# Optimization experiments

Hardware: AMD Instinct MI355X
Metric: run time of the kernel (lower is better)

Reference implementation:

```python
import jax, jax.numpy as jnp
import numpy as np
from jax import lax

B, T, F = 8, 512, 128          # batch, mel time, mel freq
DM, DS, DC, EXP, NL = 384, 16, 4, 2, 12
DI = EXP * DM                   # 768 inner width
DTR = (DM + 15) // 16           # 24, mamba_ssm dt_rank='auto'
PT = PF = 16
L = (T // PT) * (F // PF)       # 256 patches
NC = 4


def setup_inputs() -> dict:
    key = jax.random.key(0)
    ks = iter(jax.random.split(key, 24))
    def n(shape, s=0.02):
        return jax.random.normal(next(ks), shape, jnp.float32) * s
    return {
        "x": jax.random.normal(next(ks), (B, T, F), jnp.float32),
        "patch_w": n((DM, PT, PF)),
        "patch_b": jnp.zeros((DM,), jnp.float32),
        "pos_embed": n((1, L, DM)),
        "ln_g": jnp.ones((NL, DM), jnp.float32),
        "ln_b": jnp.zeros((NL, DM), jnp.float32),
        "in_proj_w": n((NL, 2 * DI, DM)),
        "conv_w": n((NL, DI, DC), 0.1),
        "conv_b": jnp.zeros((NL, DI), jnp.float32),
        "x_proj_w": n((NL, DTR + 2 * DS, DI)),
        "dt_proj_w": n((NL, DI, DTR), 0.1),
        "dt_proj_b": n((NL, DI), 0.1),
        "A_log": jnp.tile(jnp.log(jnp.arange(1, DS + 1, dtype=jnp.float32))[None, None, :], (NL, DI, 1)),
        "Dskip": jnp.ones((NL, DI), jnp.float32),
        "out_proj_w": n((NL, DM, DI)),
        "fn_g": jnp.ones((DM,), jnp.float32),
        "fn_b": jnp.zeros((DM,), jnp.float32),
        "head_w": n((NC, DM)),
        "head_b": jnp.zeros((NC,), jnp.float32),
    }


def _layernorm(x, g, b):
    m = x.mean(-1, keepdims=True)
    v = jnp.var(x, axis=-1, keepdims=True)
    return (x - m) * lax.rsqrt(v + 1e-5) * g + b


def _silu(v):
    return v * jax.nn.sigmoid(v)


def _mamba_block(x, p):
    # x: [B, L, DM]; residual Mamba block (pre-LN, dropout=identity in eval)
    ln_g, ln_b, Wi, cw, cb, Wx, Wdt, bdt, A_log, Dsk, Wo = p
    res = x
    h = _layernorm(x, ln_g, ln_b)
    xz = jnp.einsum('bld,ed->ble', h, Wi)          # [B,L,2*DI]
    u, z = jnp.split(xz, 2, axis=-1)
    # causal depthwise conv1d, kernel DC (small, unrolled)
    up = jnp.pad(u, ((0, 0), (DC - 1, 0), (0, 0)))
    u = sum(up[:, k:k + L, :] * cw[:, k] for k in range(DC)) + cb
    u = _silu(u)
    proj = jnp.einsum('bld,ed->ble', u, Wx)        # [B,L,DTR+2*DS]
    dt, Bm, Cm = jnp.split(proj, [DTR, DTR + DS], axis=-1)
    delta = jax.nn.softplus(jnp.einsum('blr,dr->bld', dt, Wdt) + bdt)  # [B,L,DI]
    A = -jnp.exp(A_log)                            # [DI, DS]
    dA = jnp.exp(delta[..., None] * A)             # [B,L,DI,DS]
    dBu = (delta * u)[..., None] * Bm[:, :, None, :]

    def step(hst, inp):
        dA_t, dBu_t, C_t = inp
        hst = dA_t * hst + dBu_t                   # [B,DI,DS]
        return hst, jnp.einsum('bdn,bn->bd', hst, C_t)

    h0 = jnp.zeros((x.shape[0], DI, DS), x.dtype)
    _, ys = lax.scan(step, h0, (dA.swapaxes(0, 1), dBu.swapaxes(0, 1), Cm.swapaxes(0, 1)))
    y = ys.swapaxes(0, 1) + u * Dsk                # [B,L,DI]
    y = y * _silu(z)
    return res + jnp.einsum('bld,ed->ble', y, Wo)


def reference(x, patch_w, patch_b, pos_embed, ln_g, ln_b, in_proj_w, conv_w, conv_b,
              x_proj_w, dt_proj_w, dt_proj_b, A_log, Dskip, out_proj_w,
              fn_g, fn_b, head_w, head_b):
    Bn = x.shape[0]
    # patch embed = non-overlapping 16x16 conv == blocked reshape + einsum
    patches = x.reshape(Bn, T // PT, PT, F // PF, PF)
    tok = jnp.einsum('bhpwq,dpq->bhwd', patches, patch_w) + patch_b
    tok = tok.reshape(Bn, L, DM) + pos_embed

    def layer(carry, p):
        return _mamba_block(carry, p), None

    tok, _ = lax.scan(layer, tok, (ln_g, ln_b, in_proj_w, conv_w, conv_b,
                                   x_proj_w, dt_proj_w, dt_proj_b, A_log, Dskip, out_proj_w))
    tok = _layernorm(tok, fn_g, fn_b)
    pooled = tok.mean(axis=1)
    return pooled @ head_w.T + head_b
```

## Files before the change

kernel.cpp:

```cpp
#include <hip/hip_runtime.h>
#include <math.h>

namespace {

constexpr int kB   = 8;
constexpr int kL   = 256;
constexpr int kTok = 2048;
constexpr int kDM  = 384;
constexpr int kDI  = 768;
constexpr int kDS  = 16;
constexpr int kDTR = 24;
constexpr int kPROJ = 56;
constexpr int kNL  = 12;

constexpr int kWIN  = 2 * kDI * kDM;
constexpr int kWOUT = kDM * kDI;
constexpr int kWX   = kPROJ * kDI;
constexpr int kWTOT = kWIN + kWOUT + kWX;

typedef float f32x4 __attribute__((ext_vector_type(4)));
typedef short short8 __attribute__((ext_vector_type(8)));

__device__ __forceinline__ float softplus_f(float x) {
  return (x > 20.f) ? x : log1pf(__expf(x));
}
__device__ __forceinline__ float silu_f(float x) {
  return x / (1.f + __expf(-x));
}
__device__ __forceinline__ unsigned short f2bf(float f) {
  union { float f; unsigned u; } v; v.f = f;
  unsigned r = v.u + 0x7FFFu + ((v.u >> 16) & 1u);
  return (unsigned short)(r >> 16);
}
__device__ __forceinline__ float bf2f(unsigned short u) {
  return __uint_as_float((unsigned)u << 16);
}

__global__ __launch_bounds__(256) void patch_gemm_k(
    const float* __restrict__ x, const float* __restrict__ Bw,
    const float* __restrict__ bias, const float* __restrict__ pos,
    float* __restrict__ C) {
  __shared__ float As[16][68];
  __shared__ float Bs[16][68];
  int tid = threadIdx.x;
  int bm = blockIdx.y * 64;
  int bn = blockIdx.x * 64;
  int lr = tid >> 2;
  int lk = (tid & 3) << 2;
  int tm = (tid >> 4) << 2;
  int tn = (tid & 15) << 2;
  float acc[4][4] = {};
  for (int k0 = 0; k0 < 256; k0 += 16) {
    {
      int token = bm + lr;
      int b = token >> 8, l = token & 255;
      int h = l >> 3, w = l & 7;
      int p = k0 >> 4;
      const float* ap = x + ((size_t)(b * 512) + h * 16 + p) * 128 + w * 16 + lk;
      float4 av = *(const float4*)ap;
      As[lk + 0][lr] = av.x; As[lk + 1][lr] = av.y;
      As[lk + 2][lr] = av.z; As[lk + 3][lr] = av.w;
    }
    {
      const float* bp = Bw + (size_t)(bn + lr) * 256 + k0 + lk;
      float4 bv = *(const float4*)bp;
      Bs[lk + 0][lr] = bv.x; Bs[lk + 1][lr] = bv.y;
      Bs[lk + 2][lr] = bv.z; Bs[lk + 3][lr] = bv.w;
    }
    __syncthreads();
    #pragma unroll
    for (int k = 0; k < 16; ++k) {
      float4 a = *(const float4*)&As[k][tm];
      float4 b = *(const float4*)&Bs[k][tn];
      float av[4] = {a.x, a.y, a.z, a.w};
      float bv[4] = {b.x, b.y, b.z, b.w};
      #pragma unroll
      for (int i = 0; i < 4; ++i)
        #pragma unroll
        for (int j = 0; j < 4; ++j)
          acc[i][j] = fmaf(av[i], bv[j], acc[i][j]);
    }
    __syncthreads();
  }
  #pragma unroll
  for (int i = 0; i < 4; ++i) {
    int row = bm + tm + i;
    #pragma unroll
    for (int j = 0; j < 4; ++j) {
      int col = bn + tn + j;
      C[(size_t)row * kDM + col] =
          acc[i][j] + bias[col] + pos[(size_t)(row & 255) * kDM + col];
    }
  }
}

__global__ __launch_bounds__(384) void lnpool_head_k(
    const float* __restrict__ in, const float* __restrict__ g,
    const float* __restrict__ bb, const float* __restrict__ hw,
    const float* __restrict__ hb, float* __restrict__ out) {
  int t = blockIdx.x, d = threadIdx.x;
  float v = in[(size_t)t * kDM + d];
  float s = v, s2 = v * v;
  #pragma unroll
  for (int m = 32; m >= 1; m >>= 1) {
    s  += __shfl_xor(s, m);
    s2 += __shfl_xor(s2, m);
  }
  __shared__ float ps[6], ps2[6];
  __shared__ float pc[6][4];
  int wv = d >> 6;
  if ((d & 63) == 0) { ps[wv] = s; ps2[wv] = s2; }
  __syncthreads();
  float S = 0.f, S2 = 0.f;
  #pragma unroll
  for (int i = 0; i < 6; ++i) { S += ps[i]; S2 += ps2[i]; }
  float mean = S * (1.f / 384.f);
  float var  = S2 * (1.f / 384.f) - mean * mean;
  float r = rsqrtf(var + 1e-5f);
  float o = (v - mean) * r * g[d] + bb[d];
  float p[4];
  #pragma unroll
  for (int c = 0; c < 4; ++c) p[c] = o * hw[(size_t)c * kDM + d];
  #pragma unroll
  for (int m = 32; m >= 1; m >>= 1) {
    #pragma unroll
    for (int c = 0; c < 4; ++c) p[c] += __shfl_xor(p[c], m);
  }
  if ((d & 63) == 0) {
    #pragma unroll
    for (int c = 0; c < 4; ++c) pc[wv][c] = p[c];
  }
  __syncthreads();
  if (d < 4) {
    float acc = 0.f;
    #pragma unroll
    for (int i = 0; i < 6; ++i) acc += pc[i][d];
    acc *= (1.f / 256.f);
    if ((t & 255) == 0) acc += hb[d];
    atomicAdd(&out[(size_t)(t >> 8) * 4 + d], acc);
  }
}

__global__ __launch_bounds__(256) void convert_all_k(
    const float* __restrict__ w_in, const float* __restrict__ w_out,
    const float* __restrict__ w_x, unsigned short* __restrict__ dst) {
  int layer = blockIdx.y;
  int tid = threadIdx.x;
  int i4 = (blockIdx.x * 256 + tid) * 4;
  if (i4 >= kWTOT) return;
  const float* src;
  int off;
  if (i4 < kWIN) { src = w_in + (size_t)layer * kWIN; off = i4; }
  else if (i4 < kWIN + kWOUT) { src = w_out + (size_t)layer * kWOUT; off = i4 - kWIN; }
  else { src = w_x + (size_t)layer * kWX; off = i4 - kWIN - kWOUT; }
  float4 v = *(const float4*)(src + off);
  unsigned short o[4] = {f2bf(v.x), f2bf(v.y), f2bf(v.z), f2bf(v.w)};
  *(uint2*)(dst + (size_t)layer * kWTOT + i4) = *(const uint2*)o;
}

__global__ __launch_bounds__(256) void inproj_ln_k(
    const float* __restrict__ tok, const unsigned short* __restrict__ Bw,
    const float* __restrict__ g, const float* __restrict__ bb,
    unsigned short* __restrict__ Cbf, float* __restrict__ proj_zero) {
  __shared__ __align__(16) unsigned short As[4][64][8];
  __shared__ __align__(16) unsigned short Bs[4][128][8];
  __shared__ float smean[64], srstd[64];
  __shared__ float sg_[kDM], sb_[kDM];
  int tid = threadIdx.x;
  int bm = blockIdx.y * 64;
  int bn = blockIdx.x * 128;
  {
    int bid = blockIdx.y * 12 + blockIdx.x;
    for (int i = bid * 256 + tid; i < kTok * kPROJ; i += 384 * 256)
      proj_zero[i] = 0.f;
  }
  for (int i = tid; i < kDM; i += 256) { sg_[i] = g[i]; sb_[i] = bb[i]; }
  {
    int r = tid >> 2, quarter = tid & 3;
    const float* rp = tok + (size_t)(bm + r) * kDM + quarter * 96;
    float s = 0.f, s2 = 0.f;
    #pragma unroll
    for (int q = 0; q < 24; ++q) {
      float4 v = ((const float4*)rp)[q];
      s  += v.x + v.y + v.z + v.w;
      s2 += v.x * v.x + v.y * v.y + v.z * v.z + v.w * v.w;
    }
    s  += __shfl_xor(s, 1);  s2 += __shfl_xor(s2, 1);
    s  += __shfl_xor(s, 2);  s2 += __shfl_xor(s2, 2);
    if (quarter == 0) {
      float mean = s * (1.f / 384.f);
      float var  = s2 * (1.f / 384.f) - mean * mean;
      smean[r] = mean;
      srstd[r] = rsqrtf(var + 1e-5f);
    }
  }
  __syncthreads();
  int wave = tid >> 6, lane = tid & 63;
  int lm = lane & 15, lq = lane >> 4;
  int wm = (wave & 1) * 32, wn = (wave >> 1) * 64;
  f32x4 acc[2][4] = {};
  for (int k0 = 0; k0 < kDM; k0 += 32) {
    int ar = tid & 63, aq = tid >> 6;
    unsigned short av[8];
    {
      float mean = smean[ar], rstd = srstd[ar];
      const float* ap = tok + (size_t)(bm + ar) * kDM + k0 + aq * 8;
      float4 v0 = ((const float4*)ap)[0];
      float4 v1 = ((const float4*)ap)[1];
      float vv[8] = {v0.x, v0.y, v0.z, v0.w, v1.x, v1.y, v1.z, v1.w};
      #pragma unroll
      for (int j = 0; j < 8; ++j) {
        int k = k0 + aq * 8 + j;
        av[j] = f2bf((vv[j] - mean) * rstd * sg_[k] + sb_[k]);
      }
    }
    int br = tid & 127, bq0 = tid >> 7, bq1 = bq0 + 2;
    uint4 b0 = *(const uint4*)(Bw + (size_t)(bn + br) * kDM + k0 + bq0 * 8);
    uint4 b1 = *(const uint4*)(Bw + (size_t)(bn + br) * kDM + k0 + bq1 * 8);
    __syncthreads();
    *(uint4*)&As[aq][ar][0]  = *(const uint4*)av;
    *(uint4*)&Bs[bq0][br][0] = b0;
    *(uint4*)&Bs[bq1][br][0] = b1;
    __syncthreads();
    short8 bfrag[4];
    #pragma unroll
    for (int ni = 0; ni < 4; ++ni)
      bfrag[ni] = *(const short8*)&Bs[lq][wn + ni * 16 + lm][0];
    #pragma unroll
    for (int mi = 0; mi < 2; ++mi) {
      short8 afrag = *(const short8*)&As[lq][wm + mi * 16 + lm][0];
      #pragma unroll
      for (int ni = 0; ni < 4; ++ni)
        acc[mi][ni] = __builtin_amdgcn_mfma_f32_16x16x32_bf16(
            afrag, bfrag[ni], acc[mi][ni], 0, 0, 0);
    }
  }
  #pragma unroll
  for (int mi = 0; mi < 2; ++mi) {
    #pragma unroll
    for (int ni = 0; ni < 4; ++ni) {
      int grow0 = bm + wm + mi * 16 + lq * 4;
      int gcol = bn + wn + ni * 16 + lm;
      #pragma unroll
      for (int r = 0; r < 4; ++r)
        Cbf[(size_t)(grow0 + r) * (2 * kDI) + gcol] = f2bf(acc[mi][ni][r]);
    }
  }
}

__global__ __launch_bounds__(256) void xproj_conv_k(
    const unsigned short* __restrict__ xz, const unsigned short* __restrict__ Bw,
    const float* __restrict__ cw, const float* __restrict__ cb,
    float* __restrict__ proj, unsigned short* __restrict__ uT_bf,
    unsigned short* __restrict__ sgT_bf) {
  __shared__ __align__(16) unsigned short As[4][64][8];
  __shared__ __align__(16) unsigned short Bs[4][64][8];
  __shared__ float scw[128][4];
  __shared__ float scb[128];
  int tid = threadIdx.x;
  int bm = blockIdx.x * 64;
  int kbase = blockIdx.y * 128;
  int wave = tid >> 6, lane = tid & 63;
  int lm = lane & 15, lq = lane >> 4;
  int wm = wave * 16;
  f32x4 acc[4] = {};

  if (tid < 128) {
    *(float4*)&scw[tid][0] = *(const float4*)(cw + (size_t)(kbase + tid) * 4);
    scb[tid] = cb[kbase + tid];
  }
  __syncthreads();

  int ar = tid & 63;
  int aq = tid >> 6;
  int t = bm + ar;
  int b = t >> 8, l = t & 255;

  for (int kt = 0; kt < 4; ++kt) {
    int k0 = kbase + kt * 32;
    int dloc = kt * 32 + aq * 8;
    int dg = kbase + dloc;
    unsigned short av[8];
    {
      float vals[4][8];
      #pragma unroll
      for (int q = 0; q < 4; ++q) {
        if (l - 3 + q >= 0) {
          uint4 r = *(const uint4*)(xz + (size_t)(t - 3 + q) * (2 * kDI) + dg);
          const unsigned short* rs = (const unsigned short*)&r;
          #pragma unroll
          for (int j = 0; j < 8; ++j) vals[q][j] = bf2f(rs[j]);
        } else {
          #pragma unroll
          for (int j = 0; j < 8; ++j) vals[q][j] = 0.f;
        }
      }
      uint4 zr = *(const uint4*)(xz + (size_t)t * (2 * kDI) + kDI + dg);
      const unsigned short* zs = (const unsigned short*)&zr;
      #pragma unroll
      for (int j = 0; j < 8; ++j) {
        float a = scb[dloc + j];
        a = fmaf(vals[0][j], scw[dloc + j][0], a);
        a = fmaf(vals[1][j], scw[dloc + j][1], a);
        a = fmaf(vals[2][j], scw[dloc + j][2], a);
        a = fmaf(vals[3][j], scw[dloc + j][3], a);
        unsigned short ub = f2bf(silu_f(a));
        av[j] = ub;
        size_t rbase = ((size_t)b * kDI + dg + j) * kL + l;
        uT_bf[rbase] = ub;
        sgT_bf[rbase] = f2bf(silu_f(bf2f(zs[j])));
      }
    }
    int br = tid & 63, bq = tid >> 6;
    uint4 b0;
    if (br < kPROJ)
      b0 = *(const uint4*)(Bw + (size_t)br * kDI + k0 + bq * 8);
    else
      b0 = make_uint4(0u, 0u, 0u, 0u);
    __syncthreads();
    *(uint4*)&As[aq][ar][0] = *(const uint4*)av;
    *(uint4*)&Bs[bq][br][0] = b0;
    __syncthreads();
    short8 afrag = *(const short8*)&As[lq][wm + lm][0];
    #pragma unroll
    for (int ni = 0; ni < 4; ++ni) {
      short8 bfrag = *(const short8*)&Bs[lq][ni * 16 + lm][0];
      acc[ni] = __builtin_amdgcn_mfma_f32_16x16x32_bf16(
          afrag, bfrag, acc[ni], 0, 0, 0);
    }
  }

  #pragma unroll
  for (int ni = 0; ni < 4; ++ni) {
    int grow0 = bm + wm + lq * 4;
    int gcol = ni * 16 + lm;
    if (gcol < kPROJ) {
      #pragma unroll
      for (int r = 0; r < 4; ++r)
        atomicAdd(&proj[(size_t)(grow0 + r) * kPROJ + gcol], acc[ni][r]);
    }
  }
}

__global__ __launch_bounds__(256) void bgemm_out_k(
    const unsigned short* __restrict__ A, int lda,
    const unsigned short* __restrict__ B, int ldb,
    float* __restrict__ C, int ldc, int Kc) {
  __shared__ __align__(16) unsigned short As[4][64][8];
  __shared__ __align__(16) unsigned short Bs[4][64][8];
  int tid = threadIdx.x;
  int bm = blockIdx.y * 64;
  int bn = blockIdx.x * 64;
  int k_begin = blockIdx.z * Kc;
  int wave = tid >> 6, lane = tid & 63;
  int lm = lane & 15, lq = lane >> 4;
  int wm = (wave & 1) * 32, wn = (wave >> 1) * 32;
  f32x4 acc[2][2] = {};

  for (int kt = 0; kt < Kc; kt += 32) {
    int k0 = k_begin + kt;
    int ar = tid & 63, aq = tid >> 6;
    uint4 a0 = *(const uint4*)(A + (size_t)(bm + ar) * lda + k0 + aq * 8);
    uint4 b0 = *(const uint4*)(B + (size_t)(bn + ar) * ldb + k0 + aq * 8);
    __syncthreads();
    *(uint4*)&As[aq][ar][0] = a0;
    *(uint4*)&Bs[aq][ar][0] = b0;
    __syncthreads();
    short8 bfrag[2];
    #pragma unroll
    for (int ni = 0; ni < 2; ++ni)
      bfrag[ni] = *(const short8*)&Bs[lq][wn + ni * 16 + lm][0];
    #pragma unroll
    for (int mi = 0; mi < 2; ++mi) {
      short8 afrag = *(const short8*)&As[lq][wm + mi * 16 + lm][0];
      #pragma unroll
      for (int ni = 0; ni < 2; ++ni)
        acc[mi][ni] = __builtin_amdgcn_mfma_f32_16x16x32_bf16(
            afrag, bfrag[ni], acc[mi][ni], 0, 0, 0);
    }
  }

  #pragma unroll
  for (int mi = 0; mi < 2; ++mi) {
    #pragma unroll
    for (int ni = 0; ni < 2; ++ni) {
      int grow0 = bm + wm + mi * 16 + lq * 4;
      int gcol = bn + wn + ni * 16 + lm;
      #pragma unroll
      for (int r = 0; r < 4; ++r)
        atomicAdd(&C[(size_t)(grow0 + r) * ldc + gcol], acc[mi][ni][r]);
    }
  }
}

__global__ __launch_bounds__(256, 3) void scansplit_k(
    const float* __restrict__ proj, const unsigned short* __restrict__ uT_bf,
    const unsigned short* __restrict__ sgT_bf, const float* __restrict__ dtw,
    const float* __restrict__ dtb, const float* __restrict__ A_log,
    const float* __restrict__ Dsk, unsigned short* __restrict__ y_bf) {
  int d0 = blockIdx.x * 4;
  int b = blockIdx.y;
  int tid = threadIdx.x;
  int dsub = tid & 3;
  int nq = (tid >> 2) & 3;
  int c = tid >> 4;
  int d = d0 + dsub;
  __shared__ float sproj[256][33];
  __shared__ float sdt[16][16][5];
  __shared__ float sh[16][16][5];
  __shared__ float sca[16][16][5];

  const float* pr0 = proj + (size_t)(b * kL) * kPROJ;

  {
    const float* rp = pr0 + (size_t)tid * kPROJ;
    #pragma unroll
    for (int q = 0; q < 6; ++q) {
      float4 v = ((const float4*)rp)[q];
      sproj[tid][q * 4 + 0] = v.x;
      sproj[tid][q * 4 + 1] = v.y;
      sproj[tid][q * 4 + 2] = v.z;
      sproj[tid][q * 4 + 3] = v.w;
    }
  }

  float Av2[4];
  {
    const float kLog2e = 1.44269504088896340736f;
    float4 v = *(const float4*)(A_log + (size_t)d * kDS + nq * 4);
    Av2[0] = -__expf(v.x) * kLog2e;
    Av2[1] = -__expf(v.y) * kLog2e;
    Av2[2] = -__expf(v.z) * kLog2e;
    Av2[3] = -__expf(v.w) * kLog2e;
  }
  float bdt = dtb[d];
  float Dv = Dsk[d];

  float wdt[24];
  {
    const float* wp = dtw + (size_t)d * kDTR;
    #pragma unroll
    for (int q = 0; q < 6; ++q) {
      float4 v = ((const float4*)wp)[q];
      wdt[q * 4 + 0] = v.x; wdt[q * 4 + 1] = v.y;
      wdt[q * 4 + 2] = v.z; wdt[q * 4 + 3] = v.w;
    }
  }

  union { uint4 v[2]; unsigned short s[16]; } uu;
  {
    const unsigned short* up = uT_bf + ((size_t)b * kDI + d) * kL + c * 16;
    uu.v[0] = ((const uint4*)up)[0];
    uu.v[1] = ((const uint4*)up)[1];
  }

  __syncthreads();

  #pragma unroll
  for (int i = 0; i < 4; ++i) {
    int tok = c * 16 + nq * 4 + i;
    float acc = bdt;
    #pragma unroll
    for (int r = 0; r < 24; ++r) acc = fmaf(sproj[tok][r], wdt[r], acc);
    sdt[c][nq * 4 + i][dsub] = softplus_f(acc);
  }
  __syncthreads();

  {
    const float* rp = pr0 + (size_t)tid * kPROJ + 24;
    #pragma unroll
    for (int q = 0; q < 8; ++q) {
      float4 v = ((const float4*)rp)[q];
      sproj[tid][q * 4 + 0] = v.x;
      sproj[tid][q * 4 + 1] = v.y;
      sproj[tid][q * 4 + 2] = v.z;
      sproj[tid][q * 4 + 3] = v.w;
    }
  }
  __syncthreads();

  float h[4] = {};
  float S = 0.f;
  #pragma unroll
  for (int i = 0; i < 16; ++i) {
    int tok = c * 16 + i;
    float dl = sdt[c][i][dsub];
    float du = dl * bf2f(uu.s[i]);
    S += dl;
    #pragma unroll
    for (int n = 0; n < 4; ++n) {
      float a = exp2f(dl * Av2[n]);
      h[n] = fmaf(a, h[n], du * sproj[tok][nq * 4 + n]);
    }
  }
  {
    int nrow = nq * 4;
    #pragma unroll
    for (int n = 0; n < 4; ++n) {
      sh[c][nrow + n][dsub] = h[n];
      sca[c][nrow + n][dsub] = exp2f(S * Av2[n]);
    }
  }
  __syncthreads();

  float h0[4] = {};
  {
    int nrow = nq * 4;
    for (int j = 0; j < c; ++j) {
      #pragma unroll
      for (int n = 0; n < 4; ++n)
        h0[n] = fmaf(sca[j][nrow + n][dsub], h0[n], sh[j][nrow + n][dsub]);
    }
  }

  union { uint4 v[2]; unsigned short s[16]; } zz;
  zz.v[0] = make_uint4(0u, 0u, 0u, 0u);
  zz.v[1] = make_uint4(0u, 0u, 0u, 0u);
  if (nq == 0) {
    const unsigned short* sp = sgT_bf + ((size_t)b * kDI + d) * kL + c * 16;
    zz.v[0] = ((const uint4*)sp)[0];
    zz.v[1] = ((const uint4*)sp)[1];
  }

  unsigned short* yp = y_bf + (size_t)(b * kL + c * 16) * kDI + d;
  #pragma unroll
  for (int i = 0; i < 16; ++i) {
    int tok = c * 16 + i;
    float dl = sdt[c][i][dsub];
    float uv = bf2f(uu.s[i]);
    float du = dl * uv;
    float yv = 0.f;
    #pragma unroll
    for (int n = 0; n < 4; ++n) {
      float a = exp2f(dl * Av2[n]);
      h0[n] = fmaf(a, h0[n], du * sproj[tok][nq * 4 + n]);
      yv = fmaf(h0[n], sproj[tok][16 + nq * 4 + n], yv);
    }
    yv += __shfl_xor(yv, 4);
    yv += __shfl_xor(yv, 8);
    if (nq == 0) yp[(size_t)i * kDI] = f2bf((yv + uv * Dv) * bf2f(zz.s[i]));
  }
}

}

extern "C" void kernel_launch(void* const* d_in, const int* in_sizes, int n_in,
                              void* d_out, int out_size, void* d_ws, size_t ws_size,
                              hipStream_t stream) {
  (void)in_sizes; (void)n_in; (void)out_size; (void)ws_size;
  const float* x        = (const float*)d_in[0];
  const float* patch_w  = (const float*)d_in[1];
  const float* patch_b  = (const float*)d_in[2];
  const float* pos      = (const float*)d_in[3];
  const float* ln_g     = (const float*)d_in[4];
  const float* ln_b     = (const float*)d_in[5];
  const float* in_w     = (const float*)d_in[6];
  const float* conv_w   = (const float*)d_in[7];
  const float* conv_b   = (const float*)d_in[8];
  const float* xproj_w  = (const float*)d_in[9];
  const float* dtproj_w = (const float*)d_in[10];
  const float* dtproj_b = (const float*)d_in[11];
  const float* A_log    = (const float*)d_in[12];
  const float* Dskip    = (const float*)d_in[13];
  const float* out_w    = (const float*)d_in[14];
  const float* fn_g     = (const float*)d_in[15];
  const float* fn_b     = (const float*)d_in[16];
  const float* head_w   = (const float*)d_in[17];
  const float* head_b   = (const float*)d_in[18];
  float* out = (float*)d_out;

  float* ws = (float*)d_ws;
  float* tok    = ws; ws += kTok * kDM;
  float* proj   = ws; ws += kTok * kPROJ;
  unsigned short* xz_bf  = (unsigned short*)ws; ws += kTok * 2 * kDI / 2;
  unsigned short* uT_bf  = (unsigned short*)ws; ws += kTok * kDI / 2;
  unsigned short* sgT_bf = (unsigned short*)ws; ws += kTok * kDI / 2;
  unsigned short* y_bf   = (unsigned short*)ws; ws += kTok * kDI / 2;
  unsigned short* w_bf   = (unsigned short*)ws; ws += (size_t)kNL * kWTOT / 2;

  convert_all_k<<<dim3(kWTOT / 4 / 256, kNL), 256, 0, stream>>>(
      in_w, out_w, xproj_w, w_bf);

  patch_gemm_k<<<dim3(6, 32), 256, 0, stream>>>(x, patch_w, patch_b, pos, tok);

  for (int layer = 0; layer < kNL; ++layer) {
    const unsigned short* wl = w_bf + (size_t)layer * kWTOT;
    inproj_ln_k<<<dim3(12, 32), 256, 0, stream>>>(
        tok, wl, ln_g + layer * kDM, ln_b + layer * kDM, xz_bf, proj);
    xproj_conv_k<<<dim3(32, 6), 256, 0, stream>>>(
        xz_bf, wl + kWIN + kWOUT, conv_w + layer * kDI * 4,
        conv_b + layer * kDI, proj, uT_bf, sgT_bf);
    scansplit_k<<<dim3(kDI / 4, kB), 256, 0, stream>>>(
        proj, uT_bf, sgT_bf, dtproj_w + (size_t)layer * kDI * kDTR,
        dtproj_b + layer * kDI, A_log + (size_t)layer * kDI * kDS,
        Dskip + layer * kDI, y_bf);
    bgemm_out_k<<<dim3(6, 32, 4), 256, 0, stream>>>(
        y_bf, kDI, wl + kWIN, kDI, tok, kDM, kDI / 4);
  }

  lnpool_head_k<<<kTok, kDM, 0, stream>>>(tok, fn_g, fn_b, head_w, head_b, out);
}
```

Measured before the change: 1.171 ms.

## Drop shared-memory proj staging in scan kernel, read B/C/dt inputs directly from global

```diff
diff --git a/kernel.cpp b/kernel.cpp
--- a/kernel.cpp
+++ b/kernel.cpp
@@ -393,7 +393,7 @@
   }
 }
 
-__global__ __launch_bounds__(256, 3) void scansplit_k(
+__global__ __launch_bounds__(256, 5) void scansplit_k(
     const float* __restrict__ proj, const unsigned short* __restrict__ uT_bf,
     const unsigned short* __restrict__ sgT_bf, const float* __restrict__ dtw,
     const float* __restrict__ dtb, const float* __restrict__ A_log,
@@ -405,24 +405,9 @@
   int nq = (tid >> 2) & 3;
   int c = tid >> 4;
   int d = d0 + dsub;
-  __shared__ float sproj[256][33];
   __shared__ float sdt[16][16][5];
   __shared__ float sh[16][16][5];
   __shared__ float sca[16][16][5];
-
-  const float* pr0 = proj + (size_t)(b * kL) * kPROJ;
-
-  {
-    const float* rp = pr0 + (size_t)tid * kPROJ;
-    #pragma unroll
-    for (int q = 0; q < 6; ++q) {
-      float4 v = ((const float4*)rp)[q];
-      sproj[tid][q * 4 + 0] = v.x;
-      sproj[tid][q * 4 + 1] = v.y;
-      sproj[tid][q * 4 + 2] = v.z;
-      sproj[tid][q * 4 + 3] = v.w;
-    }
-  }
 
   float Av2[4];
   {
@@ -436,8 +421,10 @@
   float bdt = dtb[d];
   float Dv = Dsk[d];
 
-  float wdt[24];
-  {
+  const float* pr = proj + ((size_t)(b * kL) + c * 16) * kPROJ;
+
+  {
+    float wdt[24];
     const float* wp = dtw + (size_t)d * kDTR;
     #pragma unroll
     for (int q = 0; q < 6; ++q) {
@@ -445,6 +432,20 @@
       wdt[q * 4 + 0] = v.x; wdt[q * 4 + 1] = v.y;
       wdt[q * 4 + 2] = v.z; wdt[q * 4 + 3] = v.w;
     }
+    #pragma unroll
+    for (int i = 0; i < 4; ++i) {
+      const float* p = pr + (size_t)(nq * 4 + i) * kPROJ;
+      float acc = bdt;
+      #pragma unroll
+      for (int q = 0; q < 6; ++q) {
+        float4 v = ((const float4*)p)[q];
+        acc = fmaf(v.x, wdt[q * 4 + 0], acc);
+        acc = fmaf(v.y, wdt[q * 4 + 1], acc);
+        acc = fmaf(v.z, wdt[q * 4 + 2], acc);
+        acc = fmaf(v.w, wdt[q * 4 + 3], acc);
+      }
+      sdt[c][nq * 4 + i][dsub] = softplus_f(acc);
+    }
   }
 
   union { uint4 v[2]; unsigned short s[16]; } uu;
@@ -453,44 +454,20 @@
     uu.v[0] = ((const uint4*)up)[0];
     uu.v[1] = ((const uint4*)up)[1];
   }
-
   __syncthreads();
 
-  #pragma unroll
-  for (int i = 0; i < 4; ++i) {
-    int tok = c * 16 + nq * 4 + i;
-    float acc = bdt;
-    #pragma unroll
-    for (int r = 0; r < 24; ++r) acc = fmaf(sproj[tok][r], wdt[r], acc);
-    sdt[c][nq * 4 + i][dsub] = softplus_f(acc);
-  }
-  __syncthreads();
-
-  {
-    const float* rp = pr0 + (size_t)tid * kPROJ + 24;
-    #pragma unroll
-    for (int q = 0; q < 8; ++q) {
-      float4 v = ((const float4*)rp)[q];
-      sproj[tid][q * 4 + 0] = v.x;
-      sproj[tid][q * 4 + 1] = v.y;
-      sproj[tid][q * 4 + 2] = v.z;
-      sproj[tid][q * 4 + 3] = v.w;
-    }
-  }
-  __syncthreads();
-
-  float h[4] = {};
-  float S = 0.f;
+  float h[4] = {}, ca[4] = {1.f, 1.f, 1.f, 1.f};
   #pragma unroll
   for (int i = 0; i < 16; ++i) {
-    int tok = c * 16 + i;
     float dl = sdt[c][i][dsub];
     float du = dl * bf2f(uu.s[i]);
-    S += dl;
+    float4 Bq = *(const float4*)(pr + (size_t)i * kPROJ + 24 + nq * 4);
+    float Bv[4] = {Bq.x, Bq.y, Bq.z, Bq.w};
     #pragma unroll
     for (int n = 0; n < 4; ++n) {
       float a = exp2f(dl * Av2[n]);
-      h[n] = fmaf(a, h[n], du * sproj[tok][nq * 4 + n]);
+      h[n] = fmaf(a, h[n], du * Bv[n]);
+      ca[n] *= a;
     }
   }
   {
@@ -498,7 +475,7 @@
     #pragma unroll
     for (int n = 0; n < 4; ++n) {
       sh[c][nrow + n][dsub] = h[n];
-      sca[c][nrow + n][dsub] = exp2f(S * Av2[n]);
+      sca[c][nrow + n][dsub] = ca[n];
     }
   }
   __syncthreads();
@@ -525,16 +502,20 @@
   unsigned short* yp = y_bf + (size_t)(b * kL + c * 16) * kDI + d;
   #pragma unroll
   for (int i = 0; i < 16; ++i) {
-    int tok = c * 16 + i;
     float dl = sdt[c][i][dsub];
     float uv = bf2f(uu.s[i]);
     float du = dl * uv;
+    const float* p = pr + (size_t)i * kPROJ + 24 + nq * 4;
+    float4 Bq = *(const float4*)p;
+    float4 Cq = *(const float4*)(p + 16);
+    float Bv[4] = {Bq.x, Bq.y, Bq.z, Bq.w};
+    float Cv[4] = {Cq.x, Cq.y, Cq.z, Cq.w};
     float yv = 0.f;
     #pragma unroll
     for (int n = 0; n < 4; ++n) {
       float a = exp2f(dl * Av2[n]);
-      h0[n] = fmaf(a, h0[n], du * sproj[tok][nq * 4 + n]);
-      yv = fmaf(h0[n], sproj[tok][16 + nq * 4 + n], yv);
+      h0[n] = fmaf(a, h0[n], du * Bv[n]);
+      yv = fmaf(h0[n], Cv[n], yv);
     }
     yv += __shfl_xor(yv, 4);
     yv += __shfl_xor(yv, 8);
```

New measurement: 1.126 ms. 1.04x faster.
